# Performance work log

Hardware: AMD Instinct MI355X
Metric: run time of the kernel (lower is better)

Reference implementation:

```python
import jax, jax.numpy as jnp
import numpy as np

B, S, D, H, L, E, F, K, V = 4, 1024, 768, 12, 2, 8, 3072, 2, 50257
HD = D // H
EPS = 1e-6
N_TIME, N_LOC, N_ROAD, N_WEATHER = 288, 1000, 10, 8


def rmsnorm(x, w):
    return x / jnp.sqrt(jnp.mean(x * x, axis=-1, keepdims=True) + EPS) * w


def rope_cache(seq_len, dim):
    inv_freq = 1.0 / (10000.0 ** (jnp.arange(0, dim, 2, dtype=jnp.float32) / dim))
    freqs = jnp.arange(seq_len, dtype=jnp.float32)[:, None] * inv_freq[None, :]
    emb = jnp.concatenate([freqs, freqs], axis=-1)  # [S, HD]
    return jnp.cos(emb), jnp.sin(emb)


def rotate_half(x):
    h = x.shape[-1] // 2
    return jnp.concatenate([-x[..., h:], x[..., :h]], axis=-1)


def attention(x, Wq, Wk, Wv, Wo, cos, sin):
    b, s, d = x.shape
    def heads(w):
        return (x @ w).reshape(b, s, H, HD).transpose(0, 2, 1, 3)  # [B,H,S,HD]
    q, k, v = heads(Wq), heads(Wk), heads(Wv)
    c, sn = cos[None, None], sin[None, None]
    q = q * c + rotate_half(q) * sn
    k = k * c + rotate_half(k) * sn
    scores = jnp.einsum('bhqd,bhkd->bhqk', q, k) / jnp.sqrt(jnp.float32(HD))
    mask = jnp.tril(jnp.ones((s, s), dtype=bool))
    scores = jnp.where(mask[None, None], scores, jnp.finfo(scores.dtype).min)
    probs = jax.nn.softmax(scores, axis=-1)
    out = jnp.einsum('bhqk,bhkd->bhqd', probs, v)
    return out.transpose(0, 2, 1, 3).reshape(b, s, d) @ Wo


def moe(x, router_w, Wg, Wu, Wd):
    # x: [T, D]; top-k routed SwiGLU experts, combine weights renormalized over top-k
    probs = jax.nn.softmax(x @ router_w, axis=-1)              # [T, E]
    w, idx = jax.lax.top_k(probs, K)                           # [T, K]
    w = w / jnp.sum(w, axis=-1, keepdims=True)
    onehot = jax.nn.one_hot(idx, E, dtype=x.dtype)             # [T, K, E]
    combine = jnp.sum(onehot * w[..., None], axis=1)           # [T, E]
    out = jnp.zeros_like(x)
    for e in range(E):  # small fixed expert count
        h = jax.nn.silu(x @ Wg[e]) * (x @ Wu[e])               # [T, F]
        out = out + combine[:, e, None] * (h @ Wd[e])
    usage = jnp.mean(jnp.sum(onehot, axis=1), axis=0)          # [E]
    aux = jnp.sum(usage * jnp.mean(probs, axis=0)) * E
    return out, aux


def setup_inputs() -> dict:
    key = jax.random.key(0)
    ks = jax.random.split(key, 40)
    p = lambda i, shape: 0.02 * jax.random.normal(ks[i], shape, dtype=jnp.float32)
    inp = {}
    inp['input_ids'] = jax.random.randint(ks[0], (B, S), 0, V)
    inp['time_slots'] = jax.random.randint(ks[1], (B, 1), 0, N_TIME)
    inp['day_of_week'] = jax.random.randint(ks[2], (B, 1), 0, 7)
    inp['month'] = jax.random.randint(ks[3], (B, 1), 0, 12)
    inp['is_holiday'] = jax.random.randint(ks[4], (B, 1), 0, 2)
    inp['location_ids'] = jax.random.randint(ks[5], (B, 1), 0, N_LOC)
    inp['road_types'] = jax.random.randint(ks[6], (B, 1), 0, N_ROAD)
    inp['weather_states'] = jax.random.randint(ks[7], (B, 1), 0, N_WEATHER)
    inp['word_emb'] = p(8, (V, D))
    inp['time_emb'] = p(9, (N_TIME, D // 4))
    inp['dow_emb'] = p(10, (7, D // 4))
    inp['month_emb'] = p(11, (12, D // 4))
    inp['hol_emb'] = p(12, (2, D // 4))
    inp['loc_emb'] = p(13, (N_LOC, D // 2))
    inp['road_emb'] = p(14, (N_ROAD, D // 4))
    inp['weather_emb'] = p(15, (N_WEATHER, D // 4))
    inp['proj_w'] = p(16, (3 * D, D))
    inp['proj_b'] = jnp.zeros((D,), dtype=jnp.float32)
    inp['emb_norm_w'] = jnp.ones((D,), dtype=jnp.float32)
    inp['norm1_w'] = jnp.ones((L, D), dtype=jnp.float32)
    inp['Wq'] = p(17, (L, D, D))
    inp['Wk'] = p(18, (L, D, D))
    inp['Wv'] = p(19, (L, D, D))
    inp['Wo'] = p(20, (L, D, D))
    inp['norm2_w'] = jnp.ones((L, D), dtype=jnp.float32)
    inp['router_w'] = p(21, (L, D, E))
    inp['Wg'] = p(22, (L, E, D, F))
    inp['Wu'] = p(23, (L, E, D, F))
    inp['Wd'] = p(24, (L, E, F, D))
    inp['final_norm_w'] = jnp.ones((D,), dtype=jnp.float32)
    return inp


def reference(input_ids, time_slots, day_of_week, month, is_holiday, location_ids,
              road_types, weather_states, word_emb, time_emb, dow_emb, month_emb,
              hol_emb, loc_emb, road_emb, weather_emb, proj_w, proj_b, emb_norm_w,
              norm1_w, Wq, Wk, Wv, Wo, norm2_w, router_w, Wg, Wu, Wd, final_norm_w):
    b, s = input_ids.shape
    we = word_emb[input_ids]                                                  # [B,S,D]
    te = jnp.concatenate([time_emb[time_slots], dow_emb[day_of_week],
                          month_emb[month], hol_emb[is_holiday]], axis=-1)    # [B,1,D]
    le = loc_emb[location_ids]                                                # [B,1,D/2]
    ce = jnp.concatenate([road_emb[road_types], weather_emb[weather_states]], axis=-1)
    te = jnp.broadcast_to(te, (b, s, D))
    le = jnp.broadcast_to(le, (b, s, D // 2))
    ce = jnp.broadcast_to(ce, (b, s, D // 2))
    x = jnp.concatenate([we, te, le, ce], axis=-1) @ proj_w + proj_b          # [B,S,D]
    x = rmsnorm(x, emb_norm_w)
    cos, sin = rope_cache(s, HD)
    aux_total = jnp.float32(0.0)
    for l in range(L):
        x = x + attention(rmsnorm(x, norm1_w[l]), Wq[l], Wk[l], Wv[l], Wo[l], cos, sin)
        m, aux = moe(rmsnorm(x, norm2_w[l]).reshape(b * s, D),
                     router_w[l], Wg[l], Wu[l], Wd[l])
        x = x + m.reshape(b, s, D)
        aux_total = aux_total + aux
    x = rmsnorm(x, final_norm_w)
    return x, aux_total
```

## Files before the change

### kernel.cpp

```cpp
#include <hip/hip_runtime.h>
#include <math.h>


#define TTOK 4096
#define FDIM 3072
#define MAXSLOT 9216

typedef __attribute__((ext_vector_type(8))) short short8;
typedef __attribute__((ext_vector_type(4))) float f32x4;

__device__ __forceinline__ float bf2f(unsigned short u) {
  return __uint_as_float(((unsigned int)u) << 16);
}
__device__ __forceinline__ unsigned short f2bf(float f) {
  unsigned int u = __float_as_uint(f);
  u += 0x7fffu + ((u >> 16) & 1u);
  return (unsigned short)(u >> 16);
}
__device__ __forceinline__ void split3f(float a, unsigned short& h, unsigned short& m,
                                        unsigned short& l) {
  h = f2bf(a);
  float r = a - bf2f(h);
  m = f2bf(r);
  r -= bf2f(m);
  l = f2bf(r);
}
__device__ __forceinline__ void split2f(float a, unsigned short& h, unsigned short& m) {
  h = f2bf(a);
  m = f2bf(a - bf2f(h));
}
__device__ __forceinline__ void gload16(const void* g, void* l) {
  __builtin_amdgcn_global_load_lds((const __attribute__((address_space(1))) unsigned int*)g,
                                   (__attribute__((address_space(3))) unsigned int*)l, 16, 0, 0);
}

#define MFMA_TERM(ACC, PA, PB)                                                              \
  _Pragma("unroll") for (int i_ = 0; i_ < 4; ++i_)                                          \
      _Pragma("unroll") for (int j_ = 0; j_ < 4; ++j_)                                      \
          ACC[i_][j_] = __builtin_amdgcn_mfma_f32_16x16x32_bf16(af[PA][i_], bf[PB][j_],     \
                                                                ACC[i_][j_], 0, 0, 0);
#define MFMA_SPLIT3(ACC)  \
  MFMA_TERM(ACC, 0, 2) MFMA_TERM(ACC, 2, 0) MFMA_TERM(ACC, 1, 1) \
  MFMA_TERM(ACC, 0, 1) MFMA_TERM(ACC, 1, 0) MFMA_TERM(ACC, 0, 0)
#define MFMA_SPLIT2(ACC)  \
  MFMA_TERM(ACC, 0, 1) MFMA_TERM(ACC, 1, 0) MFMA_TERM(ACC, 0, 0)


__global__ void rope_cache_k(float* __restrict__ cosb, float* __restrict__ sinb) {
  int s = blockIdx.x, i = threadIdx.x;
  float inv = powf(10000.0f, -(float)i / 32.0f);
  float a = (float)s * inv;
  cosb[s * 32 + i] = cosf(a);
  sinb[s * 32 + i] = sinf(a);
}

__global__ void build_ctx_k(const int* ts, const int* dow, const int* mon, const int* hol,
                            const int* loc, const int* road, const int* wth,
                            const float* te, const float* de, const float* me, const float* he,
                            const float* le, const float* re, const float* we,
                            float* __restrict__ ctx) {
  int b = blockIdx.x;
  int j = blockIdx.y * 256 + threadIdx.x;
  float v;
  if (j < 192)       v = te[ts[b] * 192 + j];
  else if (j < 384)  v = de[dow[b] * 192 + (j - 192)];
  else if (j < 576)  v = me[mon[b] * 192 + (j - 384)];
  else if (j < 768)  v = he[hol[b] * 192 + (j - 576)];
  else if (j < 1152) v = le[loc[b] * 384 + (j - 768)];
  else if (j < 1344) v = re[road[b] * 192 + (j - 1152)];
  else               v = we[wth[b] * 192 + (j - 1344)];
  ctx[b * 1536 + j] = v;
}

__global__ void build_bias_k(const float* __restrict__ ctx, const float* __restrict__ pw,
                             const float* __restrict__ pb, float* __restrict__ biasB) {
  int b = blockIdx.x;
  int d = blockIdx.y * 256 + threadIdx.x;
  float s = pb[d];
  const float* cb = ctx + b * 1536;
  for (int j = 0; j < 1536; ++j) s += cb[j] * pw[(size_t)(768 + j) * 768 + d];
  biasB[b * 768 + d] = s;
}

__global__ void tconv3_k(const float* __restrict__ src, unsigned short* __restrict__ dst,
                         size_t dPS, int K, int N, size_t sstride, size_t dstride) {
  __shared__ float tile[32][33];
  src += (size_t)blockIdx.z * sstride;
  size_t dbase = (size_t)blockIdx.z * dstride;
  int n0 = blockIdx.x * 32, k0 = blockIdx.y * 32;
  int tx = threadIdx.x, ty = threadIdx.y;
  #pragma unroll
  for (int r = 0; r < 4; ++r)
    tile[ty + r * 8][tx] = src[(size_t)(k0 + ty + r * 8) * N + n0 + tx];
  __syncthreads();
  #pragma unroll
  for (int r = 0; r < 4; ++r) {
    int n = n0 + ty + r * 8;
    unsigned short h, m, lo;
    split3f(tile[tx][ty + r * 8], h, m, lo);
    size_t di = dbase + (size_t)n * K + k0 + tx;
    dst[di] = h; dst[di + dPS] = m; dst[di + 2 * dPS] = lo;
  }
}

__global__ void tconv2_k(const float* __restrict__ src, unsigned short* __restrict__ dst,
                         size_t dPS, int K, int N, size_t sstride, size_t dstride) {
  __shared__ float tile[32][33];
  src += (size_t)blockIdx.z * sstride;
  size_t dbase = (size_t)blockIdx.z * dstride;
  int n0 = blockIdx.x * 32, k0 = blockIdx.y * 32;
  int tx = threadIdx.x, ty = threadIdx.y;
  #pragma unroll
  for (int r = 0; r < 4; ++r)
    tile[ty + r * 8][tx] = src[(size_t)(k0 + ty + r * 8) * N + n0 + tx];
  __syncthreads();
  #pragma unroll
  for (int r = 0; r < 4; ++r) {
    int n = n0 + ty + r * 8;
    unsigned short h, m;
    split2f(tile[tx][ty + r * 8], h, m);
    size_t di = dbase + (size_t)n * K + k0 + tx;
    dst[di] = h; dst[di + dPS] = m;
  }
}

__global__ void tconv_k(const float* __restrict__ src, unsigned short* __restrict__ dst,
                        int K, int N, size_t sstride, size_t dstride) {
  __shared__ unsigned short tile[32][33];
  src += (size_t)blockIdx.z * sstride;
  unsigned short* d = dst + (size_t)blockIdx.z * dstride;
  int n0 = blockIdx.x * 32, k0 = blockIdx.y * 32;
  int tx = threadIdx.x, ty = threadIdx.y;
  #pragma unroll
  for (int r = 0; r < 4; ++r)
    tile[ty + r * 8][tx] = f2bf(src[(size_t)(k0 + ty + r * 8) * N + n0 + tx]);
  __syncthreads();
  #pragma unroll
  for (int r = 0; r < 4; ++r) {
    int n = n0 + ty + r * 8;
    d[(size_t)n * K + k0 + tx] = tile[tx][ty + r * 8];
  }
}

__global__ void gconv3_k(const float* __restrict__ we, const int* __restrict__ ids,
                         unsigned short* __restrict__ x3, size_t pPS) {
  int t = blockIdx.x;
  int d = threadIdx.x << 2;
  float4 v = *(const float4*)(we + (size_t)ids[t] * 768 + d);
  ushort4 vh, vm, vl;
  split3f(v.x, vh.x, vm.x, vl.x);
  split3f(v.y, vh.y, vm.y, vl.y);
  split3f(v.z, vh.z, vm.z, vl.z);
  split3f(v.w, vh.w, vm.w, vl.w);
  size_t o = (size_t)t * 768 + d;
  *(ushort4*)(x3 + o) = vh;
  *(ushort4*)(x3 + pPS + o) = vm;
  *(ushort4*)(x3 + 2 * pPS + o) = vl;
}

template <int OUT>
__global__ __launch_bounds__(256) void rmsnorm_k(const float* __restrict__ xin,
                                                 const float* __restrict__ w,
                                                 float* __restrict__ yf,
                                                 unsigned short* __restrict__ yb, size_t pPS) {
  int t = blockIdx.x;
  int tid = threadIdx.x;
  const float* xr = xin + (size_t)t * 768;
  float v0 = xr[tid], v1 = xr[tid + 256], v2 = xr[tid + 512];
  float ss = v0 * v0 + v1 * v1 + v2 * v2;
  #pragma unroll
  for (int o = 32; o > 0; o >>= 1) ss += __shfl_xor(ss, o);
  __shared__ float wss[4];
  if ((tid & 63) == 0) wss[tid >> 6] = ss;
  __syncthreads();
  float tot = wss[0] + wss[1] + wss[2] + wss[3];
  float inv = 1.0f / sqrtf(tot / 768.0f + 1e-6f);
  float o0 = v0 * inv * w[tid], o1 = v1 * inv * w[tid + 256], o2 = v2 * inv * w[tid + 512];
  if (OUT != 1) {
    float* yr = yf + (size_t)t * 768;
    yr[tid] = o0; yr[tid + 256] = o1; yr[tid + 512] = o2;
  }
  if (OUT == 1 || OUT == 2) {
    unsigned short* yr = yb + (size_t)t * 768;
    unsigned short h, m;
    split2f(o0, h, m); yr[tid] = h;       yr[tid + pPS] = m;
    split2f(o1, h, m); yr[tid + 256] = h; yr[tid + 256 + pPS] = m;
    split2f(o2, h, m); yr[tid + 512] = h; yr[tid + 512 + pPS] = m;
  }
  if (OUT == 3) {
    unsigned short* yr = yb + (size_t)t * 768;
    yr[tid] = f2bf(o0); yr[tid + 256] = f2bf(o1); yr[tid + 512] = f2bf(o2);
  }
}

__global__ __launch_bounds__(256) void rope_apply_k(float* __restrict__ qkv,
                                                    const float* __restrict__ cosb,
                                                    const float* __restrict__ sinb) {
  int idx = blockIdx.x * 256 + threadIdx.x;
  int j = idx & 31;
  int hh = (idx >> 5) % 12;
  int t = idx / 384;
  int s = t & 1023;
  float c = cosb[s * 32 + j], sn = sinb[s * 32 + j];
  size_t base = (size_t)t * 2304 + hh * 64 + j;
  float q1 = qkv[base], q2 = qkv[base + 32];
  qkv[base]      = q1 * c - q2 * sn;
  qkv[base + 32] = q2 * c + q1 * sn;
  size_t kb = base + 768;
  float k1 = qkv[kb], k2 = qkv[kb + 32];
  qkv[kb]      = k1 * c - k2 * sn;
  qkv[kb + 32] = k2 * c + k1 * sn;
}

template <int EPI>
__global__ __launch_bounds__(256) void gemm3(const unsigned short* __restrict__ A, size_t aPS,
                                             const unsigned short* __restrict__ BT, size_t bPS,
                                             float* __restrict__ Cf, int N, int K,
                                             const float* __restrict__ rowBias) {
  __shared__ __align__(16) unsigned short As[3][4096];
  __shared__ __align__(16) unsigned short Bs[3][4096];
  int tid = threadIdx.x, w = tid >> 6, l = tid & 63, lr = l & 15, lg = l >> 4;
  int m0 = blockIdx.y * 128, n0 = blockIdx.x * 128;
  size_t aoff = (size_t)(m0 + 32 * w + lr) * K + lg * 8;
// ... 21 lines not shown
      for (int i = 0; i < 4; ++i) {
        af[p][i] = *(const short8*)(&As[p][(wr * 4 + i) * 512 + l * 8]);
        bf[p][i] = *(const short8*)(&Bs[p][(wc * 4 + i) * 512 + l * 8]);
      }
    MFMA_SPLIT3(acc)
    __syncthreads();
  }
  int colb = n0 + wc * 64 + lr;
  int rowb = m0 + wr * 64 + lg * 4;
  #pragma unroll
  for (int i = 0; i < 4; ++i)
    #pragma unroll
    for (int j = 0; j < 4; ++j) {
      int col = colb + j * 16;
      #pragma unroll
      for (int r = 0; r < 4; ++r) {
        int row = rowb + i * 16 + r;
        size_t idx = (size_t)row * N + col;
        float v = acc[i][j][r];
        if (EPI == 0)      Cf[idx] = v;
        else if (EPI == 2) Cf[idx] += v;
        else               Cf[idx] = v + rowBias[(row >> 10) * 768 + col];
      }
    }
}

template <int EPI>
__global__ __launch_bounds__(256) void gemm2(const unsigned short* __restrict__ A, size_t aPS,
                                             const unsigned short* __restrict__ BT, size_t bPS,
                                             float* __restrict__ Cf, int N, int K) {
  __shared__ __align__(16) unsigned short As[2][4096];
  __shared__ __align__(16) unsigned short Bs[2][4096];
  int tid = threadIdx.x, w = tid >> 6, l = tid & 63, lr = l & 15, lg = l >> 4;
  int m0 = blockIdx.y * 128, n0 = blockIdx.x * 128;
  size_t aoff = (size_t)(m0 + 32 * w + lr) * K + lg * 8;
  size_t boff = (size_t)(n0 + 32 * w + lr) * K + lg * 8;
  size_t aoff1 = aoff + (size_t)16 * K, boff1 = boff + (size_t)16 * K;
  f32x4 acc[4][4];
  #pragma unroll
  for (int i = 0; i < 4; ++i)
    #pragma unroll
    for (int j = 0; j < 4; ++j) acc[i][j] = (f32x4){0.f, 0.f, 0.f, 0.f};
  int wr = w >> 1, wc = w & 1;
  for (int k0 = 0; k0 < K; k0 += 32) {
    #pragma unroll
    for (int p = 0; p < 2; ++p) {
      gload16(A + p * aPS + aoff + k0,  &As[p][1024 * w]);
      gload16(A + p * aPS + aoff1 + k0, &As[p][1024 * w + 512]);
      gload16(BT + p * bPS + boff + k0,  &Bs[p][1024 * w]);
      gload16(BT + p * bPS + boff1 + k0, &Bs[p][1024 * w + 512]);
    }
    __syncthreads();
    short8 af[2][4], bf[2][4];
    #pragma unroll
    for (int p = 0; p < 2; ++p)
      #pragma unroll
      for (int i = 0; i < 4; ++i) {
        af[p][i] = *(const short8*)(&As[p][(wr * 4 + i) * 512 + l * 8]);
        bf[p][i] = *(const short8*)(&Bs[p][(wc * 4 + i) * 512 + l * 8]);
      }
    MFMA_SPLIT2(acc)
    __syncthreads();
  }
  int colb = n0 + wc * 64 + lr;
  int rowb = m0 + wr * 64 + lg * 4;
  #pragma unroll
  for (int i = 0; i < 4; ++i)
    #pragma unroll
    for (int j = 0; j < 4; ++j) {
      int col = colb + j * 16;
      #pragma unroll
      for (int r = 0; r < 4; ++r) {
        int row = rowb + i * 16 + r;
        size_t idx = (size_t)row * N + col;
        float v = acc[i][j][r];
        if (EPI == 0) Cf[idx] = v;
        else          Cf[idx] += v;
      }
    }
}

template <int FUSE>
__global__ __launch_bounds__(256) void gemm2_gu(const unsigned short* __restrict__ X3, size_t xPS,
    const unsigned short* __restrict__ W2, size_t wPS, float* __restrict__ outb,
    const float* __restrict__ gin, const int* __restrict__ slot_token,
    const int* __restrict__ offs, const unsigned short* __restrict__ zp) {
  __shared__ __align__(16) unsigned short As[2][4096];
  __shared__ __align__(16) unsigned short Bs[2][4096];
  int sb = blockIdx.y * 128;
  if (sb >= offs[8]) return;
  int e = 0;
  #pragma unroll
  for (int i = 1; i < 8; ++i) if (sb >= offs[i]) e = i;
  int tid = threadIdx.x, w = tid >> 6, l = tid & 63, lr = l & 15, lg = l >> 4;
  int n0 = blockIdx.x * 128;
  const unsigned short* WE = W2 + (size_t)e * FDIM * 768;
  int t0 = slot_token[sb + 32 * w + lr];
  int t1 = slot_token[sb + 32 * w + 16 + lr];
  const unsigned short* a0[2];
  const unsigned short* a1[2];
  #pragma unroll
  for (int p = 0; p < 2; ++p) {
    a0[p] = (t0 < 0 ? zp : X3 + p * xPS + (size_t)t0 * 768) + lg * 8;
    a1[p] = (t1 < 0 ? zp : X3 + p * xPS + (size_t)t1 * 768) + lg * 8;
  }
  size_t boff = (size_t)(n0 + 32 * w + lr) * 768 + lg * 8;
  size_t boff1 = boff + (size_t)16 * 768;
  f32x4 acc[4][4];
  #pragma unroll
  for (int i = 0; i < 4; ++i)
    #pragma unroll
    for (int j = 0; j < 4; ++j) acc[i][j] = (f32x4){0.f, 0.f, 0.f, 0.f};
  int wr = w >> 1, wc = w & 1;
  for (int k0 = 0; k0 < 768; k0 += 32) {
    #pragma unroll
    for (int p = 0; p < 2; ++p) {
      gload16(a0[p] + k0, &As[p][1024 * w]);
      gload16(a1[p] + k0, &As[p][1024 * w + 512]);
      gload16(WE + p * wPS + boff + k0,  &Bs[p][1024 * w]);
      gload16(WE + p * wPS + boff1 + k0, &Bs[p][1024 * w + 512]);
    }
    __syncthreads();
    short8 af[2][4], bf[2][4];
    #pragma unroll
    for (int p = 0; p < 2; ++p)
      #pragma unroll
      for (int i = 0; i < 4; ++i) {
        af[p][i] = *(const short8*)(&As[p][(wr * 4 + i) * 512 + l * 8]);
        bf[p][i] = *(const short8*)(&Bs[p][(wc * 4 + i) * 512 + l * 8]);
      }
    MFMA_SPLIT2(acc)
    __syncthreads();
  }
  int colb = n0 + wc * 64 + lr;
  int rowb = sb + wr * 64 + lg * 4;
  #pragma unroll
  for (int i = 0; i < 4; ++i)
    #pragma unroll
    for (int j = 0; j < 4; ++j) {
      int col = colb + j * 16;
      #pragma unroll
      for (int r = 0; r < 4; ++r) {
        size_t idx = (size_t)(rowb + i * 16 + r) * FDIM + col;
        float v = acc[i][j][r];
        if (FUSE == 0) outb[idx] = v;
        else {
          float g = gin[idx];
          outb[idx] = g / (1.0f + expf(-g)) * v;
        }
      }
    }
}

__global__ __launch_bounds__(256) void gemm2_dn(const float* __restrict__ hbf,
    const unsigned short* __restrict__ W2, size_t wPS, float* __restrict__ ob,
    const int* __restrict__ offs) {
  __shared__ __align__(16) unsigned short As[2][4096];
  __shared__ __align__(16) unsigned short Bs[2][4096];
  int sb = blockIdx.y * 128;
  if (sb >= offs[8]) return;
  int e = 0;
  #pragma unroll
  for (int i = 1; i < 8; ++i) if (sb >= offs[i]) e = i;
  int tid = threadIdx.x, w = tid >> 6, l = tid & 63, lr = l & 15, lg = l >> 4;
  int n0 = blockIdx.x * 128;
  const unsigned short* WE = W2 + (size_t)e * 768 * FDIM;
  size_t boff = (size_t)(n0 + 32 * w + lr) * FDIM + lg * 8;
  size_t boff1 = boff + (size_t)16 * FDIM;
  const float* ha0 = hbf + (size_t)(sb + 32 * w + lr) * FDIM + lg * 8;
  const float* ha1 = ha0 + (size_t)16 * FDIM;
  f32x4 acc[4][4];
  #pragma unroll
  for (int i = 0; i < 4; ++i)
    #pragma unroll
    for (int j = 0; j < 4; ++j) acc[i][j] = (f32x4){0.f, 0.f, 0.f, 0.f};
  int wr = w >> 1, wc = w & 1;
  for (int k0 = 0; k0 < FDIM; k0 += 32) {
    #pragma unroll
    for (int p = 0; p < 2; ++p) {
      gload16(WE + p * wPS + boff + k0,  &Bs[p][1024 * w]);
      gload16(WE + p * wPS + boff1 + k0, &Bs[p][1024 * w + 512]);
    }
    {
      float4 v0 = *(const float4*)(ha0 + k0);
      float4 v1 = *(const float4*)(ha0 + k0 + 4);
      float va[8] = {v0.x, v0.y, v0.z, v0.w, v1.x, v1.y, v1.z, v1.w};
      short8 sh, sm;
      #pragma unroll
      for (int q = 0; q < 8; ++q) {
        unsigned short a, b;
        split2f(va[q], a, b);
        sh[q] = (short)a; sm[q] = (short)b;
      }
      *(short8*)(&As[0][1024 * w + l * 8]) = sh;
      *(short8*)(&As[1][1024 * w + l * 8]) = sm;
      v0 = *(const float4*)(ha1 + k0);
      v1 = *(const float4*)(ha1 + k0 + 4);
      float vb[8] = {v0.x, v0.y, v0.z, v0.w, v1.x, v1.y, v1.z, v1.w};
      #pragma unroll
      for (int q = 0; q < 8; ++q) {
        unsigned short a, b;
        split2f(vb[q], a, b);
        sh[q] = (short)a; sm[q] = (short)b;
      }
      *(short8*)(&As[0][1024 * w + 512 + l * 8]) = sh;
      *(short8*)(&As[1][1024 * w + 512 + l * 8]) = sm;
    }
    __syncthreads();
    short8 af[2][4], bf[2][4];
    #pragma unroll
    for (int p = 0; p < 2; ++p)
      #pragma unroll
      for (int i = 0; i < 4; ++i) {
        af[p][i] = *(const short8*)(&As[p][(wr * 4 + i) * 512 + l * 8]);
        bf[p][i] = *(const short8*)(&Bs[p][(wc * 4 + i) * 512 + l * 8]);
      }
    MFMA_SPLIT2(acc)
    __syncthreads();
  }
  int colb = n0 + wc * 64 + lr;
  int rowb = sb + wr * 64 + lg * 4;
  #pragma unroll
  for (int i = 0; i < 4; ++i)
    #pragma unroll
    for (int j = 0; j < 4; ++j) {
      int col = colb + j * 16;
      #pragma unroll
      for (int r = 0; r < 4; ++r)
        ob[(size_t)(rowb + i * 16 + r) * 768 + col] = acc[i][j][r];
    }
}

__global__ __launch_bounds__(256) void gemm_gu2(const unsigned short* __restrict__ xnb,
    const unsigned short* __restrict__ wgT, const unsigned short* __restrict__ wuT,
    unsigned short* __restrict__ gub, const int* __restrict__ slot_token,
    const int* __restrict__ offs, const unsigned short* __restrict__ zp) {
  __shared__ __align__(16) unsigned short As[4096], Bs[4096];
  int sb = blockIdx.y * 128;
  if (sb >= offs[8]) return;
  int e = 0;
  #pragma unroll
  for (int i = 1; i < 8; ++i) if (sb >= offs[i]) e = i;
  int tid = threadIdx.x, w = tid >> 6, l = tid & 63, lr = l & 15, lg = l >> 4;
  int n0 = blockIdx.x * 128;
  int nl = (n0 < FDIM) ? n0 : (n0 - FDIM);
  const unsigned short* WE = ((n0 < FDIM) ? wgT : wuT) + (size_t)e * FDIM * 768;
  unsigned short* OB = (n0 < FDIM) ? gub : (gub + (size_t)MAXSLOT * FDIM);
  int t0 = slot_token[sb + 32 * w + lr];
  int t1 = slot_token[sb + 32 * w + 16 + lr];
  const unsigned short* ga0 = (t0 < 0 ? zp : xnb + (size_t)t0 * 768) + lg * 8;
  const unsigned short* ga1 = (t1 < 0 ? zp : xnb + (size_t)t1 * 768) + lg * 8;
  const unsigned short* gb0 = WE + (size_t)(nl + 32 * w + lr) * 768 + lg * 8;
  const unsigned short* gb1 = gb0 + 16 * 768;
  f32x4 acc[4][4];
  #pragma unroll
  for (int i = 0; i < 4; ++i)
    #pragma unroll
    for (int j = 0; j < 4; ++j) acc[i][j] = (f32x4){0.f, 0.f, 0.f, 0.f};
  int wr = w >> 1, wc = w & 1;
  for (int k0 = 0; k0 < 768; k0 += 32) {
    gload16(ga0 + k0, As + 1024 * w);
    gload16(ga1 + k0, As + 1024 * w + 512);
    gload16(gb0 + k0, Bs + 1024 * w);
    gload16(gb1 + k0, Bs + 1024 * w + 512);
    __syncthreads();
    short8 af[4], bf[4];
    #pragma unroll
    for (int i = 0; i < 4; ++i) af[i] = *(const short8*)(As + (wr * 4 + i) * 512 + l * 8);
    #pragma unroll
    for (int j = 0; j < 4; ++j) bf[j] = *(const short8*)(Bs + (wc * 4 + j) * 512 + l * 8);
    #pragma unroll
    for (int i = 0; i < 4; ++i)
      #pragma unroll
      for (int j = 0; j < 4; ++j)
        acc[i][j] = __builtin_amdgcn_mfma_f32_16x16x32_bf16(af[i], bf[j], acc[i][j], 0, 0, 0);
    __syncthreads();
  }
  int colb = nl + wc * 64 + lr;
  int rowb = sb + wr * 64 + lg * 4;
  #pragma unroll
  for (int i = 0; i < 4; ++i)
    #pragma unroll
    for (int j = 0; j < 4; ++j) {
      int col = colb + j * 16;
      #pragma unroll
      for (int r = 0; r < 4; ++r)
        OB[(size_t)(rowb + i * 16 + r) * FDIM + col] = f2bf(acc[i][j][r]);
    }
}

__global__ void silu_mul_k(const unsigned short* __restrict__ gub,
                           unsigned short* __restrict__ hb) {
  size_t i = ((size_t)blockIdx.x * 256 + threadIdx.x) * 8;
  const unsigned short* u = gub + (size_t)MAXSLOT * FDIM;
  ushort4 g0 = *(const ushort4*)(gub + i);
  ushort4 g1 = *(const ushort4*)(gub + i + 4);
  ushort4 u0 = *(const ushort4*)(u + i);
  ushort4 u1 = *(const ushort4*)(u + i + 4);
  float gf[8] = {bf2f(g0.x), bf2f(g0.y), bf2f(g0.z), bf2f(g0.w),
                 bf2f(g1.x), bf2f(g1.y), bf2f(g1.z), bf2f(g1.w)};
  float uf[8] = {bf2f(u0.x), bf2f(u0.y), bf2f(u0.z), bf2f(u0.w),
                 bf2f(u1.x), bf2f(u1.y), bf2f(u1.z), bf2f(u1.w)};
  ushort4 h0, h1;
  h0.x = f2bf(gf[0] / (1.0f + expf(-gf[0])) * uf[0]);
  h0.y = f2bf(gf[1] / (1.0f + expf(-gf[1])) * uf[1]);
  h0.z = f2bf(gf[2] / (1.0f + expf(-gf[2])) * uf[2]);
  h0.w = f2bf(gf[3] / (1.0f + expf(-gf[3])) * uf[3]);
  h1.x = f2bf(gf[4] / (1.0f + expf(-gf[4])) * uf[4]);
  h1.y = f2bf(gf[5] / (1.0f + expf(-gf[5])) * uf[5]);
  h1.z = f2bf(gf[6] / (1.0f + expf(-gf[6])) * uf[6]);
  h1.w = f2bf(gf[7] / (1.0f + expf(-gf[7])) * uf[7]);
  *(ushort4*)(hb + i) = h0;
  *(ushort4*)(hb + i + 4) = h1;
}

__global__ __launch_bounds__(256) void gemm_d(const unsigned short* __restrict__ hb,
    const unsigned short* __restrict__ wdT, unsigned short* __restrict__ ob,
    const int* __restrict__ offs) {
  __shared__ __align__(16) unsigned short As[4096], Bs[4096];
  int sb = blockIdx.y * 128;
  if (sb >= offs[8]) return;
  int e = 0;
  #pragma unroll
  for (int i = 1; i < 8; ++i) if (sb >= offs[i]) e = i;
  int tid = threadIdx.x, w = tid >> 6, l = tid & 63, lr = l & 15, lg = l >> 4;
  int n0 = blockIdx.x * 128;
  const unsigned short* ga0 = hb + (size_t)(sb + 32 * w + lr) * FDIM + lg * 8;
  const unsigned short* ga1 = ga0 + (size_t)16 * FDIM;
  const unsigned short* WdE = wdT + (size_t)e * 768 * FDIM;
  const unsigned short* gb0 = WdE + (size_t)(n0 + 32 * w + lr) * FDIM + lg * 8;
  const unsigned short* gb1 = gb0 + (size_t)16 * FDIM;
  f32x4 acc[4][4];
  #pragma unroll
  for (int i = 0; i < 4; ++i)
    #pragma unroll
    for (int j = 0; j < 4; ++j) acc[i][j] = (f32x4){0.f, 0.f, 0.f, 0.f};
  int wr = w >> 1, wc = w & 1;
  for (int k0 = 0; k0 < FDIM; k0 += 32) {
    gload16(ga0 + k0, As + 1024 * w);
    gload16(ga1 + k0, As + 1024 * w + 512);
    gload16(gb0 + k0, Bs + 1024 * w);
    gload16(gb1 + k0, Bs + 1024 * w + 512);
    __syncthreads();
    short8 af[4], bf[4];
    #pragma unroll
    for (int i = 0; i < 4; ++i) af[i] = *(const short8*)(As + (wr * 4 + i) * 512 + l * 8);
    #pragma unroll
    for (int j = 0; j < 4; ++j) bf[j] = *(const short8*)(Bs + (wc * 4 + j) * 512 + l * 8);
    #pragma unroll
    for (int i = 0; i < 4; ++i)
      #pragma unroll
      for (int j = 0; j < 4; ++j)
        acc[i][j] = __builtin_amdgcn_mfma_f32_16x16x32_bf16(af[i], bf[j], acc[i][j], 0, 0, 0);
    __syncthreads();
  }
  int colb = n0 + wc * 64 + lr;
  int rowb = sb + wr * 64 + lg * 4;
  #pragma unroll
  for (int i = 0; i < 4; ++i)
    #pragma unroll
    for (int j = 0; j < 4; ++j) {
      int col = colb + j * 16;
      #pragma unroll
      for (int r = 0; r < 4; ++r)
        ob[(size_t)(rowb + i * 16 + r) * 768 + col] = f2bf(acc[i][j][r]);
    }
}

__global__ __launch_bounds__(256) void attn_k(const float* __restrict__ qkv,
                                              unsigned short* __restrict__ ax2, size_t pPS) {
  int pr = blockIdx.x, h = blockIdx.y, b = blockIdx.z;
  int tid = threadIdx.x;
  int ty4 = (tid >> 4) << 2, tx4 = (tid & 15) << 2;
  __shared__ float qs[64][68];
  __shared__ float kps[64][68];
  __shared__ float vs[64][68];
  int lr = tid >> 2;
  int lc = (tid & 3) << 4;
  for (int half = 0; half < 2; ++half) {
    int qt = half ? (15 - pr) : pr;
    int q0 = qt << 6;
    size_t qbase = ((size_t)(b * 1024 + q0 + lr)) * 2304 + h * 64 + lc;
    #pragma unroll
    for (int i = 0; i < 4; ++i) {
      float4 v = *(const float4*)(qkv + qbase + 4 * i);
      qs[lc + 4 * i + 0][lr] = v.x;
      qs[lc + 4 * i + 1][lr] = v.y;
      qs[lc + 4 * i + 2][lr] = v.z;
      qs[lc + 4 * i + 3][lr] = v.w;
    }
    float acc[4][4];
    float m[4], l[4];
    #pragma unroll
    for (int i = 0; i < 4; ++i) {
      m[i] = -3.0e38f; l[i] = 0.0f;
      #pragma unroll
      for (int j = 0; j < 4; ++j) acc[i][j] = 0.0f;
    }
    for (int kt = 0; kt <= qt; ++kt) {
      int k0 = kt << 6;
      __syncthreads();
      size_t kb = ((size_t)(b * 1024 + k0 + lr)) * 2304 + 768 + h * 64 + lc;
      #pragma unroll
      for (int i = 0; i < 4; ++i) {
        float4 kv = *(const float4*)(qkv + kb + 4 * i);
        kps[lc + 4 * i + 0][lr] = kv.x;
        kps[lc + 4 * i + 1][lr] = kv.y;
        kps[lc + 4 * i + 2][lr] = kv.z;
        kps[lc + 4 * i + 3][lr] = kv.w;
// ... 153 lines not shown

__global__ void moe_fill_k(const int* __restrict__ tk_idx, const int* __restrict__ offs,
                           int* __restrict__ fill, int* __restrict__ slot_token,
                           int* __restrict__ tk_slot) {
  int i = blockIdx.x * 256 + threadIdx.x;
  int e = tk_idx[i];
  int pos = atomicAdd(&fill[e], 1);
  int slot = offs[e] + pos;
  slot_token[slot] = i >> 1;
  tk_slot[i] = slot;
}

template <int BF>
__global__ void moe_combine_k(float* __restrict__ x, const void* __restrict__ osv,
                              const int* __restrict__ tk_slot, const float* __restrict__ tk_w) {
  int t = blockIdx.x;
  int d = threadIdx.x << 2;
  int s0 = tk_slot[t * 2], s1 = tk_slot[t * 2 + 1];
  float w0 = tk_w[t * 2], w1 = tk_w[t * 2 + 1];
  float a0, a1, a2, a3, b0, b1, b2, b3;
  if (BF == 0) {
    const float* os = (const float*)osv;
    float4 a = *(const float4*)(os + (size_t)s0 * 768 + d);
    float4 b = *(const float4*)(os + (size_t)s1 * 768 + d);
    a0 = a.x; a1 = a.y; a2 = a.z; a3 = a.w;
    b0 = b.x; b1 = b.y; b2 = b.z; b3 = b.w;
  } else {
    const unsigned short* os = (const unsigned short*)osv;
    ushort4 a = *(const ushort4*)(os + (size_t)s0 * 768 + d);
    ushort4 b = *(const ushort4*)(os + (size_t)s1 * 768 + d);
    a0 = bf2f(a.x); a1 = bf2f(a.y); a2 = bf2f(a.z); a3 = bf2f(a.w);
    b0 = bf2f(b.x); b1 = bf2f(b.y); b2 = bf2f(b.z); b3 = bf2f(b.w);
  }
  float4 c = *(const float4*)(x + (size_t)t * 768 + d);
  c.x += w0 * a0 + w1 * b0;
  c.y += w0 * a1 + w1 * b1;
  c.z += w0 * a2 + w1 * b2;
  c.w += w0 * a3 + w1 * b3;
  *(float4*)(x + (size_t)t * 768 + d) = c;
}

__global__ void write_aux_k(const float* __restrict__ aux, float* __restrict__ out) {
  out[0] = aux[0];
}


extern "C" void kernel_launch(void* const* d_in, const int* in_sizes, int n_in,
                              void* d_out, int out_size, void* d_ws, size_t ws_size,
                              hipStream_t stream) {
  const int* input_ids      = (const int*)d_in[0];
  const int* time_slots     = (const int*)d_in[1];
  const int* day_of_week    = (const int*)d_in[2];
  const int* month          = (const int*)d_in[3];
  const int* is_holiday     = (const int*)d_in[4];
  const int* location_ids   = (const int*)d_in[5];
  const int* road_types     = (const int*)d_in[6];
  const int* weather_states = (const int*)d_in[7];
  const float* word_emb     = (const float*)d_in[8];
  const float* time_emb     = (const float*)d_in[9];
  const float* dow_emb      = (const float*)d_in[10];
  const float* month_emb    = (const float*)d_in[11];
  const float* hol_emb      = (const float*)d_in[12];
  const float* loc_emb      = (const float*)d_in[13];
  const float* road_emb     = (const float*)d_in[14];
  const float* weather_emb  = (const float*)d_in[15];
  const float* proj_w       = (const float*)d_in[16];
  const float* proj_b       = (const float*)d_in[17];
  const float* emb_norm_w   = (const float*)d_in[18];
  const float* norm1_w      = (const float*)d_in[19];
  const float* Wq           = (const float*)d_in[20];
  const float* Wk           = (const float*)d_in[21];
  const float* Wv           = (const float*)d_in[22];
  const float* Wo           = (const float*)d_in[23];
  const float* norm2_w      = (const float*)d_in[24];
  const float* router_w     = (const float*)d_in[25];
  const float* Wg           = (const float*)d_in[26];
  const float* Wu           = (const float*)d_in[27];
  const float* Wd           = (const float*)d_in[28];
  const float* final_norm_w = (const float*)d_in[29];
  float* out = (float*)d_out;

  const size_t TD = (size_t)TTOK * 768;
  const size_t REG = (size_t)MAXSLOT * FDIM * 4;
  char* base = (char*)d_ws;
  auto carve = [&](size_t bytes) { char* p = base; base += (bytes + 255) & ~(size_t)255; return p; };
  float* x    = (float*)carve(TD * 4);
  float* xn   = (float*)carve(TD * 4);
  float* cosb = (float*)carve(32768 * 4);
  float* sinb = (float*)carve(32768 * 4);
  float* ctx  = (float*)carve(4 * 1536 * 4);
  float* biasB= (float*)carve(4 * 768 * 4);
  float* tkw  = (float*)carve(8192 * 4);
  float* psum = (float*)carve(64);
  float* auxa = (float*)carve(64);
  int* cnt    = (int*)carve(64);
  int* fill   = (int*)carve(64);
  int* offs   = (int*)carve(64);
  int* tk_idx = (int*)carve(8192 * 4);
  int* tk_slot= (int*)carve(8192 * 4);
  int* slot_token = (int*)carve(MAXSLOT * 4);
  unsigned short* zp = (unsigned short*)carve(4096);
  unsigned short* xnb3 = (unsigned short*)carve(3 * TD * 2);
  char* QAH = carve(REG);
  char* GT  = carve(REG);
  char* Wr  = carve(REG);
  float* qkv = (float*)QAH;
  unsigned short* ax2 = (unsigned short*)(QAH + (size_t)TTOK * 2304 * 4);
  float* hbf = (float*)QAH;
  unsigned short* hb16 = (unsigned short*)QAH;
  float* gtmp = (float*)GT;
  float* obf = (float*)GT;
  unsigned short* gu16 = (unsigned short*)GT;
  unsigned short* ob16 = (unsigned short*)GT;
  unsigned short* wpl = (unsigned short*)Wr;

  const size_t PS_D = (size_t)768 * 768;
  const size_t PS_QKV = (size_t)2304 * 768;
  const size_t PS_E = (size_t)8 * FDIM * 768;

  hipMemsetAsync(auxa, 0, 64, stream);
  hipMemsetAsync(zp, 0, 4096, stream);
  rope_cache_k<<<dim3(1024), dim3(32), 0, stream>>>(cosb, sinb);
  build_ctx_k<<<dim3(4, 6), dim3(256), 0, stream>>>(time_slots, day_of_week, month, is_holiday,
      location_ids, road_types, weather_states, time_emb, dow_emb, month_emb, hol_emb,
      loc_emb, road_emb, weather_emb, ctx);
  build_bias_k<<<dim3(4, 3), dim3(256), 0, stream>>>(ctx, proj_w, proj_b, biasB);
  tconv3_k<<<dim3(24, 24, 1), dim3(32, 8), 0, stream>>>(proj_w, wpl, PS_D, 768, 768, 0, 0);
  gconv3_k<<<dim3(TTOK), dim3(192), 0, stream>>>(word_emb, input_ids, xnb3, TD);
  gemm3<3><<<dim3(6, 32), dim3(256), 0, stream>>>(xnb3, TD, wpl, PS_D, xn, 768, 768, biasB);
  rmsnorm_k<0><<<dim3(TTOK), dim3(256), 0, stream>>>(xn, emb_norm_w, x, nullptr, 0);

  for (int l = 0; l < 2; ++l) {
    const float* rw = router_w + (size_t)l * 768 * 8;
    tconv2_k<<<dim3(24, 24, 1), dim3(32, 8), 0, stream>>>(Wq + (size_t)l * PS_D, wpl, PS_QKV, 768, 768, 0, 0);
    tconv2_k<<<dim3(24, 24, 1), dim3(32, 8), 0, stream>>>(Wk + (size_t)l * PS_D, wpl + PS_D, PS_QKV, 768, 768, 0, 0);
    tconv2_k<<<dim3(24, 24, 1), dim3(32, 8), 0, stream>>>(Wv + (size_t)l * PS_D, wpl + 2 * PS_D, PS_QKV, 768, 768, 0, 0);
    rmsnorm_k<1><<<dim3(TTOK), dim3(256), 0, stream>>>(x, norm1_w + l * 768, nullptr, xnb3, TD);
    gemm2<0><<<dim3(18, 32), dim3(256), 0, stream>>>(xnb3, TD, wpl, PS_QKV, qkv, 2304, 768);
    rope_apply_k<<<dim3(6144), dim3(256), 0, stream>>>(qkv, cosb, sinb);
    attn_k<<<dim3(8, 12, 4), dim3(256), 0, stream>>>(qkv, ax2, TD);
    tconv2_k<<<dim3(24, 24, 1), dim3(32, 8), 0, stream>>>(Wo + (size_t)l * PS_D, wpl, PS_D, 768, 768, 0, 0);
    gemm2<2><<<dim3(6, 32), dim3(256), 0, stream>>>(ax2, TD, wpl, PS_D, x, 768, 768);

    if (l == 0)
      rmsnorm_k<2><<<dim3(TTOK), dim3(256), 0, stream>>>(x, norm2_w, xn, xnb3, TD);
    else
      rmsnorm_k<3><<<dim3(TTOK), dim3(256), 0, stream>>>(x, norm2_w + 768, xn, xnb3, TD);
    hipMemsetAsync(cnt, 0, 64, stream);
    hipMemsetAsync(fill, 0, 64, stream);
    hipMemsetAsync(psum, 0, 64, stream);
    hipMemsetAsync(slot_token, 0xFF, MAXSLOT * 4, stream);
    router_k<<<dim3(1024), dim3(256), 0, stream>>>(xn, rw, tk_idx, tkw, cnt, psum);
    moe_offsets_k<<<dim3(1), dim3(64), 0, stream>>>(cnt, offs, psum, auxa);
    moe_fill_k<<<dim3(32), dim3(256), 0, stream>>>(tk_idx, offs, fill, slot_token, tk_slot);
    if (l == 0) {
      tconv2_k<<<dim3(96, 24, 8), dim3(32, 8), 0, stream>>>(Wg, wpl, PS_E,
          768, FDIM, (size_t)768 * FDIM, (size_t)FDIM * 768);
      gemm2_gu<0><<<dim3(24, MAXSLOT / 128), dim3(256), 0, stream>>>(xnb3, TD, wpl, PS_E,
          gtmp, nullptr, slot_token, offs, zp);
      tconv2_k<<<dim3(96, 24, 8), dim3(32, 8), 0, stream>>>(Wu, wpl, PS_E,
          768, FDIM, (size_t)768 * FDIM, (size_t)FDIM * 768);
      gemm2_gu<1><<<dim3(24, MAXSLOT / 128), dim3(256), 0, stream>>>(xnb3, TD, wpl, PS_E,
          hbf, gtmp, slot_token, offs, zp);
      tconv2_k<<<dim3(24, 96, 8), dim3(32, 8), 0, stream>>>(Wd, wpl, PS_E,
          FDIM, 768, (size_t)FDIM * 768, (size_t)768 * FDIM);
      gemm2_dn<<<dim3(6, MAXSLOT / 128), dim3(256), 0, stream>>>(hbf, wpl, PS_E, obf, offs);
      moe_combine_k<0><<<dim3(TTOK), dim3(192), 0, stream>>>(x, obf, tk_slot, tkw);
    } else {
      const float* wg1 = Wg + (size_t)8 * 768 * FDIM;
      const float* wu1 = Wu + (size_t)8 * 768 * FDIM;
      const float* wd1 = Wd + (size_t)8 * FDIM * 768;
      tconv_k<<<dim3(96, 24, 8), dim3(32, 8), 0, stream>>>(wg1, wpl,
          768, FDIM, (size_t)768 * FDIM, (size_t)FDIM * 768);
      tconv_k<<<dim3(96, 24, 8), dim3(32, 8), 0, stream>>>(wu1, wpl + PS_E,
          768, FDIM, (size_t)768 * FDIM, (size_t)FDIM * 768);
      gemm_gu2<<<dim3(48, MAXSLOT / 128), dim3(256), 0, stream>>>(xnb3, wpl, wpl + PS_E,
          gu16, slot_token, offs, zp);
      silu_mul_k<<<dim3((int)((size_t)MAXSLOT * FDIM / 2048)), dim3(256), 0, stream>>>(gu16, hb16);
      tconv_k<<<dim3(24, 96, 8), dim3(32, 8), 0, stream>>>(wd1, wpl,
          FDIM, 768, (size_t)FDIM * 768, (size_t)768 * FDIM);
      gemm_d<<<dim3(6, MAXSLOT / 128), dim3(256), 0, stream>>>(hb16, wpl, ob16, offs);
      moe_combine_k<1><<<dim3(TTOK), dim3(192), 0, stream>>>(x, ob16, tk_slot, tkw);
    }
  }

  rmsnorm_k<0><<<dim3(TTOK), dim3(256), 0, stream>>>(x, final_norm_w, out, nullptr, 0);
  write_aux_k<<<dim3(1), dim3(1), 0, stream>>>(auxa, out + TD);
}
```

Before: 2.129 ms.

## Widen transpose tiles, remap MoE GEMM blocks per XCD, store split-bf16 hidden

The weight transpose/convert kernels now use 64x64 tiles with 64x4 threads, so each thread handles 16 rows and block count drops. The MoE GEMMs switch to a 1D grid whose block index is permuted (blockIdx&7 scaled) so that consecutive blocks on each of the eight XCDs share expert weights and row tiles, aiming for better L2 locality. The layer-0 gate/up fused epilogue now writes the SiLU product as hi/lo bf16 planes. This lets the down-projection GEMM load them with gload16 instead of converting fp32 per tile, trading a larger epilogue store for a cheaper inner loop.

```diff
diff --git a/kernel.cpp b/kernel.cpp
--- a/kernel.cpp
+++ b/kernel.cpp
@@ -82,22 +82,23 @@
   biasB[b * 768 + d] = s;
 }
 
+
 __global__ void tconv3_k(const float* __restrict__ src, unsigned short* __restrict__ dst,
                          size_t dPS, int K, int N, size_t sstride, size_t dstride) {
-  __shared__ float tile[32][33];
+  __shared__ float tile[64][65];
   src += (size_t)blockIdx.z * sstride;
   size_t dbase = (size_t)blockIdx.z * dstride;
-  int n0 = blockIdx.x * 32, k0 = blockIdx.y * 32;
+  int n0 = blockIdx.x * 64, k0 = blockIdx.y * 64;
   int tx = threadIdx.x, ty = threadIdx.y;
   #pragma unroll
-  for (int r = 0; r < 4; ++r)
-    tile[ty + r * 8][tx] = src[(size_t)(k0 + ty + r * 8) * N + n0 + tx];
+  for (int r = 0; r < 16; ++r)
+    tile[ty + r * 4][tx] = src[(size_t)(k0 + ty + r * 4) * N + n0 + tx];
   __syncthreads();
   #pragma unroll
-  for (int r = 0; r < 4; ++r) {
-    int n = n0 + ty + r * 8;
+  for (int r = 0; r < 16; ++r) {
+    int n = n0 + ty + r * 4;
     unsigned short h, m, lo;
-    split3f(tile[tx][ty + r * 8], h, m, lo);
+    split3f(tile[tx][ty + r * 4], h, m, lo);
     size_t di = dbase + (size_t)n * K + k0 + tx;
     dst[di] = h; dst[di + dPS] = m; dst[di + 2 * dPS] = lo;
   }
@@ -105,20 +106,20 @@
 
 __global__ void tconv2_k(const float* __restrict__ src, unsigned short* __restrict__ dst,
                          size_t dPS, int K, int N, size_t sstride, size_t dstride) {
-  __shared__ float tile[32][33];
+  __shared__ float tile[64][65];
   src += (size_t)blockIdx.z * sstride;
   size_t dbase = (size_t)blockIdx.z * dstride;
-  int n0 = blockIdx.x * 32, k0 = blockIdx.y * 32;
+  int n0 = blockIdx.x * 64, k0 = blockIdx.y * 64;
   int tx = threadIdx.x, ty = threadIdx.y;
   #pragma unroll
-  for (int r = 0; r < 4; ++r)
-    tile[ty + r * 8][tx] = src[(size_t)(k0 + ty + r * 8) * N + n0 + tx];
+  for (int r = 0; r < 16; ++r)
+    tile[ty + r * 4][tx] = src[(size_t)(k0 + ty + r * 4) * N + n0 + tx];
   __syncthreads();
   #pragma unroll
-  for (int r = 0; r < 4; ++r) {
-    int n = n0 + ty + r * 8;
+  for (int r = 0; r < 16; ++r) {
+    int n = n0 + ty + r * 4;
     unsigned short h, m;
-    split2f(tile[tx][ty + r * 8], h, m);
+    split2f(tile[tx][ty + r * 4], h, m);
     size_t di = dbase + (size_t)n * K + k0 + tx;
     dst[di] = h; dst[di + dPS] = m;
   }
@@ -126,19 +127,19 @@
 
 __global__ void tconv_k(const float* __restrict__ src, unsigned short* __restrict__ dst,
                         int K, int N, size_t sstride, size_t dstride) {
-  __shared__ unsigned short tile[32][33];
+  __shared__ float tile[64][65];
   src += (size_t)blockIdx.z * sstride;
   unsigned short* d = dst + (size_t)blockIdx.z * dstride;
-  int n0 = blockIdx.x * 32, k0 = blockIdx.y * 32;
+  int n0 = blockIdx.x * 64, k0 = blockIdx.y * 64;
   int tx = threadIdx.x, ty = threadIdx.y;
   #pragma unroll
-  for (int r = 0; r < 4; ++r)
-    tile[ty + r * 8][tx] = f2bf(src[(size_t)(k0 + ty + r * 8) * N + n0 + tx]);
+  for (int r = 0; r < 16; ++r)
+    tile[ty + r * 4][tx] = src[(size_t)(k0 + ty + r * 4) * N + n0 + tx];
   __syncthreads();
   #pragma unroll
-  for (int r = 0; r < 4; ++r) {
-    int n = n0 + ty + r * 8;
-    d[(size_t)n * K + k0 + tx] = tile[tx][ty + r * 8];
+  for (int r = 0; r < 16; ++r) {
+    int n = n0 + ty + r * 4;
+    d[(size_t)n * K + k0 + tx] = f2bf(tile[tx][ty + r * 4]);
   }
 }
 
@@ -326,18 +327,20 @@
 
 template <int FUSE>
 __global__ __launch_bounds__(256) void gemm2_gu(const unsigned short* __restrict__ X3, size_t xPS,
-    const unsigned short* __restrict__ W2, size_t wPS, float* __restrict__ outb,
-    const float* __restrict__ gin, const int* __restrict__ slot_token,
-    const int* __restrict__ offs, const unsigned short* __restrict__ zp) {
+    const unsigned short* __restrict__ W2, size_t wPS, float* __restrict__ gout,
+    unsigned short* __restrict__ hout, size_t hPS, const float* __restrict__ gin,
+    const int* __restrict__ slot_token, const int* __restrict__ offs,
+    const unsigned short* __restrict__ zp) {
   __shared__ __align__(16) unsigned short As[2][4096];
   __shared__ __align__(16) unsigned short Bs[2][4096];
-  int sb = blockIdx.y * 128;
+  int L = ((blockIdx.x & 7) * 216) + (blockIdx.x >> 3);
+  int sb = (L % 72) * 128;
+  int n0 = (L / 72) * 128;
   if (sb >= offs[8]) return;
   int e = 0;
   #pragma unroll
   for (int i = 1; i < 8; ++i) if (sb >= offs[i]) e = i;
   int tid = threadIdx.x, w = tid >> 6, l = tid & 63, lr = l & 15, lg = l >> 4;
-  int n0 = blockIdx.x * 128;
   const unsigned short* WE = W2 + (size_t)e * FDIM * 768;
   int t0 = slot_token[sb + 32 * w + lr];
   int t1 = slot_token[sb + 32 * w + 16 + lr];
@@ -387,32 +390,36 @@
       for (int r = 0; r < 4; ++r) {
         size_t idx = (size_t)(rowb + i * 16 + r) * FDIM + col;
         float v = acc[i][j][r];
-        if (FUSE == 0) outb[idx] = v;
+        if (FUSE == 0) gout[idx] = v;
         else {
           float g = gin[idx];
-          outb[idx] = g / (1.0f + expf(-g)) * v;
+          float h = g / (1.0f + expf(-g)) * v;
+          unsigned short hh, hm;
+          split2f(h, hh, hm);
+          hout[idx] = hh; hout[idx + hPS] = hm;
         }
       }
     }
 }
 
-__global__ __launch_bounds__(256) void gemm2_dn(const float* __restrict__ hbf,
+__global__ __launch_bounds__(256) void gemm2_dn(const unsigned short* __restrict__ hpl, size_t hPS,
     const unsigned short* __restrict__ W2, size_t wPS, float* __restrict__ ob,
     const int* __restrict__ offs) {
   __shared__ __align__(16) unsigned short As[2][4096];
   __shared__ __align__(16) unsigned short Bs[2][4096];
-  int sb = blockIdx.y * 128;
+  int L = ((blockIdx.x & 7) * 54) + (blockIdx.x >> 3);
+  int sb = (L % 72) * 128;
+  int n0 = (L / 72) * 128;
   if (sb >= offs[8]) return;
   int e = 0;
   #pragma unroll
   for (int i = 1; i < 8; ++i) if (sb >= offs[i]) e = i;
   int tid = threadIdx.x, w = tid >> 6, l = tid & 63, lr = l & 15, lg = l >> 4;
-  int n0 = blockIdx.x * 128;
   const unsigned short* WE = W2 + (size_t)e * 768 * FDIM;
+  size_t aoff = (size_t)(sb + 32 * w + lr) * FDIM + lg * 8;
+  size_t aoff1 = aoff + (size_t)16 * FDIM;
   size_t boff = (size_t)(n0 + 32 * w + lr) * FDIM + lg * 8;
   size_t boff1 = boff + (size_t)16 * FDIM;
-  const float* ha0 = hbf + (size_t)(sb + 32 * w + lr) * FDIM + lg * 8;
-  const float* ha1 = ha0 + (size_t)16 * FDIM;
   f32x4 acc[4][4];
   #pragma unroll
   for (int i = 0; i < 4; ++i)
@@ -422,33 +429,10 @@
   for (int k0 = 0; k0 < FDIM; k0 += 32) {
     #pragma unroll
     for (int p = 0; p < 2; ++p) {
+      gload16(hpl + p * hPS + aoff + k0,  &As[p][1024 * w]);
+      gload16(hpl + p * hPS + aoff1 + k0, &As[p][1024 * w + 512]);
       gload16(WE + p * wPS + boff + k0,  &Bs[p][1024 * w]);
       gload16(WE + p * wPS + boff1 + k0, &Bs[p][1024 * w + 512]);
-    }
-    {
-      float4 v0 = *(const float4*)(ha0 + k0);
-      float4 v1 = *(const float4*)(ha0 + k0 + 4);
-      float va[8] = {v0.x, v0.y, v0.z, v0.w, v1.x, v1.y, v1.z, v1.w};
-      short8 sh, sm;
-      #pragma unroll
-      for (int q = 0; q < 8; ++q) {
-        unsigned short a, b;
-        split2f(va[q], a, b);
-        sh[q] = (short)a; sm[q] = (short)b;
-      }
-      *(short8*)(&As[0][1024 * w + l * 8]) = sh;
-      *(short8*)(&As[1][1024 * w + l * 8]) = sm;
-      v0 = *(const float4*)(ha1 + k0);
-      v1 = *(const float4*)(ha1 + k0 + 4);
-      float vb[8] = {v0.x, v0.y, v0.z, v0.w, v1.x, v1.y, v1.z, v1.w};
-      #pragma unroll
-      for (int q = 0; q < 8; ++q) {
-        unsigned short a, b;
-        split2f(vb[q], a, b);
-        sh[q] = (short)a; sm[q] = (short)b;
-      }
-      *(short8*)(&As[0][1024 * w + 512 + l * 8]) = sh;
-      *(short8*)(&As[1][1024 * w + 512 + l * 8]) = sm;
     }
     __syncthreads();
     short8 af[2][4], bf[2][4];
@@ -480,13 +464,14 @@
     unsigned short* __restrict__ gub, const int* __restrict__ slot_token,
     const int* __restrict__ offs, const unsigned short* __restrict__ zp) {
   __shared__ __align__(16) unsigned short As[4096], Bs[4096];
-  int sb = blockIdx.y * 128;
+  int L = ((blockIdx.x & 7) * 432) + (blockIdx.x >> 3);
+  int sb = (L % 72) * 128;
+  int n0 = (L / 72) * 128;
   if (sb >= offs[8]) return;
   int e = 0;
   #pragma unroll
   for (int i = 1; i < 8; ++i) if (sb >= offs[i]) e = i;
   int tid = threadIdx.x, w = tid >> 6, l = tid & 63, lr = l & 15, lg = l >> 4;
-  int n0 = blockIdx.x * 128;
   int nl = (n0 < FDIM) ? n0 : (n0 - FDIM);
   const unsigned short* WE = ((n0 < FDIM) ? wgT : wuT) + (size_t)e * FDIM * 768;
   unsigned short* OB = (n0 < FDIM) ? gub : (gub + (size_t)MAXSLOT * FDIM);
@@ -562,13 +547,14 @@
     const unsigned short* __restrict__ wdT, unsigned short* __restrict__ ob,
     const int* __restrict__ offs) {
   __shared__ __align__(16) unsigned short As[4096], Bs[4096];
-  int sb = blockIdx.y * 128;
+  int L = ((blockIdx.x & 7) * 54) + (blockIdx.x >> 3);
+  int sb = (L % 72) * 128;
+  int n0 = (L / 72) * 128;
   if (sb >= offs[8]) return;
   int e = 0;
   #pragma unroll
   for (int i = 1; i < 8; ++i) if (sb >= offs[i]) e = i;
   int tid = threadIdx.x, w = tid >> 6, l = tid & 63, lr = l & 15, lg = l >> 4;
-  int n0 = blockIdx.x * 128;
   const unsigned short* ga0 = hb + (size_t)(sb + 32 * w + lr) * FDIM + lg * 8;
   const unsigned short* ga1 = ga0 + (size_t)16 * FDIM;
   const unsigned short* WdE = wdT + (size_t)e * 768 * FDIM;
@@ -888,6 +874,7 @@
 
   const size_t TD = (size_t)TTOK * 768;
   const size_t REG = (size_t)MAXSLOT * FDIM * 4;
+  const size_t HPS = (size_t)MAXSLOT * FDIM;
   char* base = (char*)d_ws;
   auto carve = [&](size_t bytes) { char* p = base; base += (bytes + 255) & ~(size_t)255; return p; };
   float* x    = (float*)carve(TD * 4);
@@ -912,7 +899,7 @@
   char* Wr  = carve(REG);
   float* qkv = (float*)QAH;
   unsigned short* ax2 = (unsigned short*)(QAH + (size_t)TTOK * 2304 * 4);
-  float* hbf = (float*)QAH;
+  unsigned short* hpl = (unsigned short*)QAH;
   unsigned short* hb16 = (unsigned short*)QAH;
   float* gtmp = (float*)GT;
   float* obf = (float*)GT;
@@ -931,21 +918,21 @@
       location_ids, road_types, weather_states, time_emb, dow_emb, month_emb, hol_emb,
       loc_emb, road_emb, weather_emb, ctx);
   build_bias_k<<<dim3(4, 3), dim3(256), 0, stream>>>(ctx, proj_w, proj_b, biasB);
-  tconv3_k<<<dim3(24, 24, 1), dim3(32, 8), 0, stream>>>(proj_w, wpl, PS_D, 768, 768, 0, 0);
+  tconv3_k<<<dim3(12, 12, 1), dim3(64, 4), 0, stream>>>(proj_w, wpl, PS_D, 768, 768, 0, 0);
   gconv3_k<<<dim3(TTOK), dim3(192), 0, stream>>>(word_emb, input_ids, xnb3, TD);
   gemm3<3><<<dim3(6, 32), dim3(256), 0, stream>>>(xnb3, TD, wpl, PS_D, xn, 768, 768, biasB);
   rmsnorm_k<0><<<dim3(TTOK), dim3(256), 0, stream>>>(xn, emb_norm_w, x, nullptr, 0);
 
   for (int l = 0; l < 2; ++l) {
     const float* rw = router_w + (size_t)l * 768 * 8;
-    tconv2_k<<<dim3(24, 24, 1), dim3(32, 8), 0, stream>>>(Wq + (size_t)l * PS_D, wpl, PS_QKV, 768, 768, 0, 0);
-    tconv2_k<<<dim3(24, 24, 1), dim3(32, 8), 0, stream>>>(Wk + (size_t)l * PS_D, wpl + PS_D, PS_QKV, 768, 768, 0, 0);
-    tconv2_k<<<dim3(24, 24, 1), dim3(32, 8), 0, stream>>>(Wv + (size_t)l * PS_D, wpl + 2 * PS_D, PS_QKV, 768, 768, 0, 0);
+    tconv2_k<<<dim3(12, 12, 1), dim3(64, 4), 0, stream>>>(Wq + (size_t)l * PS_D, wpl, PS_QKV, 768, 768, 0, 0);
+    tconv2_k<<<dim3(12, 12, 1), dim3(64, 4), 0, stream>>>(Wk + (size_t)l * PS_D, wpl + PS_D, PS_QKV, 768, 768, 0, 0);
+    tconv2_k<<<dim3(12, 12, 1), dim3(64, 4), 0, stream>>>(Wv + (size_t)l * PS_D, wpl + 2 * PS_D, PS_QKV, 768, 768, 0, 0);
     rmsnorm_k<1><<<dim3(TTOK), dim3(256), 0, stream>>>(x, norm1_w + l * 768, nullptr, xnb3, TD);
     gemm2<0><<<dim3(18, 32), dim3(256), 0, stream>>>(xnb3, TD, wpl, PS_QKV, qkv, 2304, 768);
     rope_apply_k<<<dim3(6144), dim3(256), 0, stream>>>(qkv, cosb, sinb);
     attn_k<<<dim3(8, 12, 4), dim3(256), 0, stream>>>(qkv, ax2, TD);
-    tconv2_k<<<dim3(24, 24, 1), dim3(32, 8), 0, stream>>>(Wo + (size_t)l * PS_D, wpl, PS_D, 768, 768, 0, 0);
+    tconv2_k<<<dim3(12, 12, 1), dim3(64, 4), 0, stream>>>(Wo + (size_t)l * PS_D, wpl, PS_D, 768, 768, 0, 0);
     gemm2<2><<<dim3(6, 32), dim3(256), 0, stream>>>(ax2, TD, wpl, PS_D, x, 768, 768);
 
     if (l == 0)
@@ -960,32 +947,32 @@
     moe_offsets_k<<<dim3(1), dim3(64), 0, stream>>>(cnt, offs, psum, auxa);
     moe_fill_k<<<dim3(32), dim3(256), 0, stream>>>(tk_idx, offs, fill, slot_token, tk_slot);
     if (l == 0) {
-      tconv2_k<<<dim3(96, 24, 8), dim3(32, 8), 0, stream>>>(Wg, wpl, PS_E,
+      tconv2_k<<<dim3(48, 12, 8), dim3(64, 4), 0, stream>>>(Wg, wpl, PS_E,
           768, FDIM, (size_t)768 * FDIM, (size_t)FDIM * 768);
-      gemm2_gu<0><<<dim3(24, MAXSLOT / 128), dim3(256), 0, stream>>>(xnb3, TD, wpl, PS_E,
-          gtmp, nullptr, slot_token, offs, zp);
-      tconv2_k<<<dim3(96, 24, 8), dim3(32, 8), 0, stream>>>(Wu, wpl, PS_E,
+      gemm2_gu<0><<<dim3(1728), dim3(256), 0, stream>>>(xnb3, TD, wpl, PS_E,
+          gtmp, nullptr, 0, nullptr, slot_token, offs, zp);
+      tconv2_k<<<dim3(48, 12, 8), dim3(64, 4), 0, stream>>>(Wu, wpl, PS_E,
           768, FDIM, (size_t)768 * FDIM, (size_t)FDIM * 768);
-      gemm2_gu<1><<<dim3(24, MAXSLOT / 128), dim3(256), 0, stream>>>(xnb3, TD, wpl, PS_E,
-          hbf, gtmp, slot_token, offs, zp);
-      tconv2_k<<<dim3(24, 96, 8), dim3(32, 8), 0, stream>>>(Wd, wpl, PS_E,
+      gemm2_gu<1><<<dim3(1728), dim3(256), 0, stream>>>(xnb3, TD, wpl, PS_E,
+          nullptr, hpl, HPS, gtmp, slot_token, offs, zp);
+      tconv2_k<<<dim3(12, 48, 8), dim3(64, 4), 0, stream>>>(Wd, wpl, PS_E,
           FDIM, 768, (size_t)FDIM * 768, (size_t)768 * FDIM);
-      gemm2_dn<<<dim3(6, MAXSLOT / 128), dim3(256), 0, stream>>>(hbf, wpl, PS_E, obf, offs);
+      gemm2_dn<<<dim3(432), dim3(256), 0, stream>>>(hpl, HPS, wpl, PS_E, obf, offs);
       moe_combine_k<0><<<dim3(TTOK), dim3(192), 0, stream>>>(x, obf, tk_slot, tkw);
     } else {
       const float* wg1 = Wg + (size_t)8 * 768 * FDIM;
       const float* wu1 = Wu + (size_t)8 * 768 * FDIM;
       const float* wd1 = Wd + (size_t)8 * FDIM * 768;
-      tconv_k<<<dim3(96, 24, 8), dim3(32, 8), 0, stream>>>(wg1, wpl,
+      tconv_k<<<dim3(48, 12, 8), dim3(64, 4), 0, stream>>>(wg1, wpl,
           768, FDIM, (size_t)768 * FDIM, (size_t)FDIM * 768);
-      tconv_k<<<dim3(96, 24, 8), dim3(32, 8), 0, stream>>>(wu1, wpl + PS_E,
+      tconv_k<<<dim3(48, 12, 8), dim3(64, 4), 0, stream>>>(wu1, wpl + PS_E,
           768, FDIM, (size_t)768 * FDIM, (size_t)FDIM * 768);
-      gemm_gu2<<<dim3(48, MAXSLOT / 128), dim3(256), 0, stream>>>(xnb3, wpl, wpl + PS_E,
+      gemm_gu2<<<dim3(3456), dim3(256), 0, stream>>>(xnb3, wpl, wpl + PS_E,
           gu16, slot_token, offs, zp);
       silu_mul_k<<<dim3((int)((size_t)MAXSLOT * FDIM / 2048)), dim3(256), 0, stream>>>(gu16, hb16);
-      tconv_k<<<dim3(24, 96, 8), dim3(32, 8), 0, stream>>>(wd1, wpl,
+      tconv_k<<<dim3(12, 48, 8), dim3(64, 4), 0, stream>>>(wd1, wpl,
           FDIM, 768, (size_t)FDIM * 768, (size_t)768 * FDIM);
-      gemm_d<<<dim3(6, MAXSLOT / 128), dim3(256), 0, stream>>>(hb16, wpl, ob16, offs);
+      gemm_d<<<dim3(432), dim3(256), 0, stream>>>(hb16, wpl, ob16, offs);
       moe_combine_k<1><<<dim3(TTOK), dim3(192), 0, stream>>>(x, ob16, tk_slot, tkw);
     }
   }
```

Measured after the change: 2.162 ms. No clear change (+1.6%).
